# Optimization experiments

Measured on AMD Instinct MI355X. Metric: run time of the kernel, lower is better.

Reference implementation:

```python
import jax, jax.numpy as jnp
import numpy as np

NU, NI = 40000, 60000
N = NU + NI            # total nodes
DF, DL, DI = 1024, 128, 64
E = 1600000            # number of edges
SLOPE = 0.01           # torch leaky_relu default negative slope
EPS = 1e-12            # torch F.normalize eps


def _leaky(v):
    return jnp.where(v > 0, v, SLOPE * v)


def setup_inputs() -> dict:
    key = jax.random.key(0)
    ks = jax.random.split(key, 17)
    s = 0.02  # xavier-ish scale for weights
    return {
        "features": jax.random.normal(ks[0], (NI, DF), jnp.float32),
        "id_embedding": jax.random.normal(ks[1], (N, DI), jnp.float32),
        "preference": jax.random.normal(ks[2], (NU, DL), jnp.float32) * s,
        "mlp_w": jax.random.normal(ks[3], (DL, DF), jnp.float32) * s,
        "mlp_b": jnp.zeros((DL,), jnp.float32),
        "conv1_w": jax.random.normal(ks[4], (DL, DL), jnp.float32) * s,
        "lin1_w": jax.random.normal(ks[5], (DI, DL), jnp.float32) * s,
        "lin1_b": jnp.zeros((DI,), jnp.float32),
        "g1_w": jax.random.normal(ks[6], (DI, DL), jnp.float32) * s,
        "g1_b": jnp.zeros((DI,), jnp.float32),
        "conv2_w": jax.random.normal(ks[7], (DI, DI), jnp.float32) * s,
        "lin2_w": jax.random.normal(ks[8], (DI, DI), jnp.float32) * s,
        "lin2_b": jnp.zeros((DI,), jnp.float32),
        "g2_w": jax.random.normal(ks[9], (DI, DI), jnp.float32) * s,
        "g2_b": jnp.zeros((DI,), jnp.float32),
        "edge_index": jax.random.randint(ks[10], (2, E), 0, N, jnp.int32),
    }


def reference(features, id_embedding, preference, mlp_w, mlp_b,
              conv1_w, lin1_w, lin1_b, g1_w, g1_b,
              conv2_w, lin2_w, lin2_b, g2_w, g2_b, edge_index):
    src, dst = edge_index[0], edge_index[1]

    # MLP on item features, concat with user preference -> [N, DL]
    temp = features @ mlp_w.T + mlp_b
    x = jnp.concatenate([preference, temp], axis=0)
    # row-wise L2 normalize (F.normalize dim=1)
    x = x / jnp.clip(jnp.linalg.norm(x, axis=1, keepdims=True), EPS)

    # ----- layer 1 -----
    xw = x @ conv1_w                                      # [N, DL]
    h = _leaky(jax.ops.segment_sum(xw[src], dst, num_segments=N))
    x_hat = _leaky(x @ lin1_w.T + lin1_b) + id_embedding  # [N, DI]
    x = _leaky(h @ g1_w.T + g1_b + x_hat)                 # [N, DI]

    # ----- layer 2 -----
    xw = x @ conv2_w                                      # [N, DI]
    h = _leaky(jax.ops.segment_sum(xw[src], dst, num_segments=N))
    x_hat = _leaky(x @ lin2_w.T + lin2_b) + id_embedding
    x = _leaky(h @ g2_w.T + g2_b + x_hat)
    return x
```

## Files before the change

kernel.cpp:

```cpp
#include <hip/hip_runtime.h>
#include <hip/hip_bf16.h>

typedef __hip_bfloat16 bf16;
typedef __bf16 bf16x8 __attribute__((ext_vector_type(8)));
typedef float f32x4 __attribute__((ext_vector_type(4)));

#define NU 40000
#define NI 60000
#define NN 100000
#define DF 1024
#define DL 128
#define DI 64
#define NE 1600000
#define CAP 64

__device__ __forceinline__ float leaky(float v) { return v > 0.0f ? v : 0.01f * v; }

__device__ __forceinline__ unsigned short f2b(float f) {
    unsigned u = __builtin_bit_cast(unsigned, f);
    unsigned r = (u + 0x7FFFu + ((u >> 16) & 1u)) >> 16;
    return (unsigned short)r;
}
__device__ __forceinline__ bf16 tobf(float f) {
    unsigned short r = f2b(f);
    return __builtin_bit_cast(bf16, r);
}
__device__ __forceinline__ unsigned pk2(float x, float y) {
    return (unsigned)f2b(x) | ((unsigned)f2b(y) << 16);
}
__device__ __forceinline__ float b2f_lo(unsigned u) { return __builtin_bit_cast(float, u << 16); }
__device__ __forceinline__ float b2f_hi(unsigned u) { return __builtin_bit_cast(float, u & 0xffff0000u); }

template<typename T>
__device__ __forceinline__ void stage8(bf16* dst, const T* src) {
    if constexpr (sizeof(T) == 2) {
        *(uint4*)dst = *(const uint4*)src;
    } else {
        float4 a = *(const float4*)src;
        float4 b = *(const float4*)(src + 4);
        uint2 lo, hi;
        lo.x = pk2(a.x, a.y); lo.y = pk2(a.z, a.w);
        hi.x = pk2(b.x, b.y); hi.y = pk2(b.z, b.w);
        *(uint2*)dst = lo;
        *(uint2*)(dst + 4) = hi;
    }
}
__device__ __forceinline__ void zero8(bf16* dst) {
    uint4 z = {0u, 0u, 0u, 0u};
    *(uint4*)dst = z;
}

__global__ void csr_fill(const int* __restrict__ ei, int* __restrict__ cnt,
                         int* __restrict__ bucket) {
    int e = blockIdx.x * 256 + threadIdx.x;
    if (e >= NE) return;
    int s = ei[e];
    int d = ei[NE + e];
    int p = atomicAdd(&cnt[d], 1);
    if (p < CAP) bucket[d * CAP + p] = s;
}

template<int K, int M>
__global__ void transpose_kernel(const float* __restrict__ W, bf16* __restrict__ Wt) {
    int idx = blockIdx.x * 256 + threadIdx.x;
    if (idx < K * M) {
        int k = idx / M, m = idx % M;
        Wt[m * K + k] = tobf(W[k * M + m]);
    }
}

__global__ void convert_kernel(const float* __restrict__ W, bf16* __restrict__ out) {
    int i = blockIdx.x * 256 + threadIdx.x;
    float4 v = *(const float4*)(W + (size_t)i * 4);
    uint2 p;
    p.x = pk2(v.x, v.y);
    p.y = pk2(v.z, v.w);
    *(uint2*)(out + (size_t)i * 4) = p;
}

__global__ __launch_bounds__(256) void gemm1_kernel(const float* __restrict__ A,
                                                    const bf16* __restrict__ Wb,
                                                    const float* __restrict__ bias,
                                                    bf16* __restrict__ out) {
    __shared__ __align__(16) bf16 As[2][64 * 64];
    __shared__ __align__(16) bf16 Bs[2][128 * 64];
    int t = threadIdx.x;
    int wave = t >> 6, lane = t & 63, q = lane >> 4, l16 = lane & 15;
    int wm = wave >> 1, wn = wave & 1;
    int row0 = blockIdx.x * 64;

    const float* ap[2];
    const bf16* bp[4];
    int aoff[2], boff[4];
    bool aval[2];
    #pragma unroll
    for (int i = 0; i < 2; i++) {
        int slot = t + i * 256;
        int r = slot >> 3, kc = (slot & 7) * 8;
        ap[i] = A + (size_t)(row0 + r) * DF + kc;
        aval[i] = (row0 + r) < NI;
        aoff[i] = r * 64 + (((kc >> 3) ^ (r & 7)) << 3);
    }
    #pragma unroll
    for (int i = 0; i < 4; i++) {
        int slot = t + i * 256;
        int r = slot >> 3, kc = (slot & 7) * 8;
        bp[i] = Wb + (size_t)r * DF + kc;
        boff[i] = r * 64 + (((kc >> 3) ^ (r & 7)) << 3);
    }

    float4 av[2][2];
    uint4 bv[4];
    auto issue = [&](int k0) {
        #pragma unroll
        for (int i = 0; i < 2; i++) {
            if (aval[i]) {
                av[i][0] = *(const float4*)(ap[i] + k0);
                av[i][1] = *(const float4*)(ap[i] + k0 + 4);
            } else {
                av[i][0] = float4{0.f, 0.f, 0.f, 0.f};
                av[i][1] = float4{0.f, 0.f, 0.f, 0.f};
            }
        }
        #pragma unroll
        for (int i = 0; i < 4; i++) bv[i] = *(const uint4*)(bp[i] + k0);
    };
    auto commit = [&](int buf) {
        #pragma unroll
        for (int i = 0; i < 2; i++) {
            uint4 pkd;
            pkd.x = pk2(av[i][0].x, av[i][0].y);
            pkd.y = pk2(av[i][0].z, av[i][0].w);
            pkd.z = pk2(av[i][1].x, av[i][1].y);
            pkd.w = pk2(av[i][1].z, av[i][1].w);
            *(uint4*)(&As[buf][aoff[i]]) = pkd;
        }
        #pragma unroll
        for (int i = 0; i < 4; i++) *(uint4*)(&Bs[buf][boff[i]]) = bv[i];
    };

    f32x4 acc[2][4] = {};
    issue(0);
    commit(0);
    __syncthreads();
    for (int k0i = 0; k0i < 16; k0i++) {
        int buf = k0i & 1;
        if (k0i < 15) issue((k0i + 1) * 64);
        #pragma unroll
        for (int kk = 0; kk < 64; kk += 32) {
            int ch = (kk >> 3) + q;
            int ra = wm * 32 + l16;
            bf16x8 a0 = *(const bf16x8*)&As[buf][ra * 64 + ((ch ^ (ra & 7)) << 3)];
            bf16x8 a1 = *(const bf16x8*)&As[buf][(ra + 16) * 64 + ((ch ^ (ra & 7)) << 3)];
            #pragma unroll
            for (int nt = 0; nt < 4; nt++) {
                int rb = wn * 64 + nt * 16 + l16;
                bf16x8 b = *(const bf16x8*)&Bs[buf][rb * 64 + ((ch ^ (rb & 7)) << 3)];
                acc[0][nt] = __builtin_amdgcn_mfma_f32_16x16x32_bf16(a0, b, acc[0][nt], 0, 0, 0);
                acc[1][nt] = __builtin_amdgcn_mfma_f32_16x16x32_bf16(a1, b, acc[1][nt], 0, 0, 0);
            }
        }
        if (k0i < 15) {
            commit(buf ^ 1);
            __syncthreads();
        }
    }
    #pragma unroll
    for (int mt = 0; mt < 2; mt++) {
        #pragma unroll
        for (int nt = 0; nt < 4; nt++) {
            int col = wn * 64 + nt * 16 + l16;
            float bvv = bias[col];
            #pragma unroll
            for (int r = 0; r < 4; r++) {
                int row = row0 + wm * 32 + mt * 16 + q * 4 + r;
                if (row < NI) out[(size_t)row * DL + col] = tobf(acc[mt][nt][r] + bvv);
            }
        }
    }
}

__global__ __launch_bounds__(256) void norm_kernel(const float* __restrict__ pref,
                                                   const bf16* __restrict__ temp,
                                                   bf16* __restrict__ x0) {
    __shared__ float wsum[4];
    int t = threadIdx.x;
    int g = t >> 7;
    int c = t & 127;
    int row = blockIdx.x * 2 + g;
    float v = (row < NU) ? pref[(size_t)row * DL + c]
                         : (float)temp[(size_t)(row - NU) * DL + c];
    float ss = v * v;
    #pragma unroll
    for (int off = 32; off > 0; off >>= 1) ss += __shfl_down(ss, off);
    int wave = t >> 6;
    if ((t & 63) == 0) wsum[wave] = ss;
    __syncthreads();
    float tot = wsum[g * 2] + wsum[g * 2 + 1];
    float inv = 1.0f / fmaxf(sqrtf(tot), 1e-12f);
    x0[(size_t)row * DL + c] = tobf(v * inv);
}

template<typename WT, int K, int M, int EPI, typename OutT>
__global__ __launch_bounds__(256) void sgemm_kernel(const bf16* __restrict__ A,
                                                    const WT* __restrict__ Wt,
                                                    const float* __restrict__ bias,
                                                    const float* __restrict__ extra,
                                                    OutT* __restrict__ out,
                                                    int nrows) {
    __shared__ __align__(16) bf16 As[128 * K];
    __shared__ __align__(16) bf16 Ws[M * K];
    int t = threadIdx.x;
    int wave = t >> 6, lane = t & 63;
    int q = lane >> 4, l16 = lane & 15;
    int row0 = blockIdx.x * 128;
    constexpr int WSLOT = M * K / 8;
    for (int slot = t; slot < WSLOT; slot += 256)
        stage8(Ws + slot * 8, Wt + (size_t)slot * 8);
    constexpr int SLOTS = 128 * K / 8;
    for (int slot = t; slot < SLOTS; slot += 256) {
        int r = slot / (K / 8);
        int kc = (slot % (K / 8)) * 8;
        int gr = row0 + r;
        if (gr < nrows) *(uint4*)(As + r * K + kc) = *(const uint4*)(A + (size_t)gr * K + kc);
        else            zero8(As + r * K + kc);
    }
    __syncthreads();
    constexpr int NT = M / 16;
    f32x4 acc[2][NT] = {};
    #pragma unroll
    for (int kk = 0; kk < K; kk += 32) {
        bf16x8 a0 = *(const bf16x8*)(As + (wave * 32 + l16) * K + kk + q * 8);
        bf16x8 a1 = *(const bf16x8*)(As + (wave * 32 + 16 + l16) * K + kk + q * 8);
        #pragma unroll
        for (int nt = 0; nt < NT; nt++) {
            bf16x8 b = *(const bf16x8*)(Ws + (nt * 16 + l16) * K + kk + q * 8);
            acc[0][nt] = __builtin_amdgcn_mfma_f32_16x16x32_bf16(a0, b, acc[0][nt], 0, 0, 0);
            acc[1][nt] = __builtin_amdgcn_mfma_f32_16x16x32_bf16(a1, b, acc[1][nt], 0, 0, 0);
        }
    }
    #pragma unroll
    for (int mt = 0; mt < 2; mt++) {
        #pragma unroll
        for (int nt = 0; nt < NT; nt++) {
            int col = nt * 16 + l16;
            float bv = (EPI != 0) ? bias[col] : 0.0f;
            #pragma unroll
            for (int r = 0; r < 4; r++) {
                int row = row0 + wave * 32 + mt * 16 + q * 4 + r;
                if (row < nrows) {
                    float z = acc[mt][nt][r];
                    if (EPI == 1) {
                        z = leaky(z + bv) + extra[(size_t)row * M + col];
                    } else if (EPI == 2) {
                        z = leaky(z + bv + extra[(size_t)row * M + col]);
                    }
                    if constexpr (sizeof(OutT) == 2) out[(size_t)row * M + col] = tobf(z);
                    else                             out[(size_t)row * M + col] = z;
                }
            }
        }
    }
}

template<int D>
__global__ __launch_bounds__(256) void gather_kernel(const bf16* __restrict__ xw,
                                                     const int* __restrict__ cnt,
                                                     const int* __restrict__ bucket,
                                                     bf16* __restrict__ h) {
    constexpr int TPN = D / 4;
    constexpr int GP = 256 / TPN;
    __shared__ int srcs[GP][CAP];
    int g = threadIdx.x / TPN;
    int c = threadIdx.x % TPN;
    int node = blockIdx.x * GP + g;
    int deg = min(cnt[node], CAP);
    for (int i = c; i < deg; i += TPN) srcs[g][i] = bucket[node * CAP + i];
    __syncthreads();
    const uint2* x2 = (const uint2*)xw;
    float s0 = 0.0f, s1 = 0.0f, s2 = 0.0f, s3 = 0.0f;
    for (int i = 0; i < deg; i++) {
        int s = srcs[g][i];
        uint2 v = x2[(size_t)s * (D / 4) + c];
        s0 += b2f_lo(v.x); s1 += b2f_hi(v.x);
        s2 += b2f_lo(v.y); s3 += b2f_hi(v.y);
    }
    uint2 o;
    o.x = pk2(leaky(s0), leaky(s1));
    o.y = pk2(leaky(s2), leaky(s3));
    *(uint2*)(h + (size_t)node * D + c * 4) = o;
}

extern "C" void kernel_launch(void* const* d_in, const int* in_sizes, int n_in,
                              void* d_out, int out_size, void* d_ws, size_t ws_size,
                              hipStream_t stream) {
    const void* p[16];
    for (int i = 0; i < 16 && i < n_in; i++) p[i] = d_in[i];
    if (n_in == 16) {
        int n8192 = 0, n4096 = 0, n64 = 0;
        const int idx64[4] = {7, 9, 12, 14};
        const int idx4096[3] = {10, 11, 13};
        for (int i = 0; i < 16; i++) {
            switch (in_sizes[i]) {
                case 61440000: p[0] = d_in[i]; break;
                case 6400000:  p[1] = d_in[i]; break;
                case 5120000:  p[2] = d_in[i]; break;
                case 131072:   p[3] = d_in[i]; break;
                case 128:      p[4] = d_in[i]; break;
                case 16384:    p[5] = d_in[i]; break;
                case 8192:     p[n8192++ ? 8 : 6] = d_in[i]; break;
                case 64:       if (n64 < 4) p[idx64[n64++]] = d_in[i]; break;
                case 4096:     if (n4096 < 3) p[idx4096[n4096++]] = d_in[i]; break;
                case 3200000:  p[15] = d_in[i]; break;
                default: break;
            }
        }
    }
    const float* features = (const float*)p[0];
    const float* id_emb   = (const float*)p[1];
    const float* pref     = (const float*)p[2];
    const float* mlp_w    = (const float*)p[3];
    const float* mlp_b    = (const float*)p[4];
    const float* conv1_w  = (const float*)p[5];
    const float* lin1_w   = (const float*)p[6];
    const float* lin1_b   = (const float*)p[7];
    const float* g1_w     = (const float*)p[8];
    const float* g1_b     = (const float*)p[9];
    const float* conv2_w  = (const float*)p[10];
    const float* lin2_w   = (const float*)p[11];
    const float* lin2_b   = (const float*)p[12];
    const float* g2_w     = (const float*)p[13];
    const float* g2_b     = (const float*)p[14];
    const int*   ei       = (const int*)p[15];

    char* wsp = (char*)d_ws;
    size_t off = 0;
    auto alloc = [&](size_t bytes) {
        void* ptr = wsp + off;
        off += (bytes + 255) & ~(size_t)255;
        return ptr;
    };
    void* regA = alloc((size_t)NN * DL * 2);
    void* regB = alloc((size_t)NN * DL * 2);
    void* regC = alloc((size_t)NN * DL * 2);
    int*  cnt    = (int*) alloc((size_t)NN * 4);
    int*  bucket = (int*) alloc((size_t)NN * CAP * 4);
    bf16* c1t    = (bf16*)alloc((size_t)DL * DL * 2);
    bf16* c2t    = (bf16*)alloc((size_t)DI * DI * 2);

    bf16*  temp = (bf16*)regA;
    bf16*  h1   = (bf16*)regA;
    bf16*  h2   = (bf16*)regA;
    bf16*  x0   = (bf16*)regB;
    bf16*  xw2  = (bf16*)regB;
    bf16*  mwb  = (bf16*)regC;
    bf16*  xw1  = (bf16*)regC;
    float* xhat = (float*)regC;
    bf16*  x1   = (bf16*)d_out;
    float* out  = (float*)d_out;

    hipMemsetAsync(cnt, 0, (size_t)NN * 4, stream);
    csr_fill<<<NE / 256, 256, 0, stream>>>(ei, cnt, bucket);

    transpose_kernel<DL, DL><<<(DL * DL + 255) / 256, 256, 0, stream>>>(conv1_w, c1t);
    transpose_kernel<DI, DI><<<(DI * DI + 255) / 256, 256, 0, stream>>>(conv2_w, c2t);
    convert_kernel<<<(DL * DF) / 1024, 256, 0, stream>>>(mlp_w, mwb);

    gemm1_kernel<<<(NI + 63) / 64, 256, 0, stream>>>(features, mwb, mlp_b, temp);
    norm_kernel<<<NN / 2, 256, 0, stream>>>(pref, temp, x0);

    const int SG = (NN + 127) / 128;
    sgemm_kernel<bf16, DL, DL, 0, bf16><<<SG, 256, 0, stream>>>(x0, c1t, nullptr, nullptr, xw1, NN);
    gather_kernel<DL><<<NN / 8, 256, 0, stream>>>(xw1, cnt, bucket, h1);
    sgemm_kernel<float, DL, DI, 1, float><<<SG, 256, 0, stream>>>(x0, lin1_w, lin1_b, id_emb, xhat, NN);
    sgemm_kernel<float, DL, DI, 2, bf16><<<SG, 256, 0, stream>>>(h1, g1_w, g1_b, xhat, x1, NN);
    sgemm_kernel<float, DI, DI, 1, float><<<SG, 256, 0, stream>>>(x1, lin2_w, lin2_b, id_emb, xhat, NN);
    sgemm_kernel<bf16, DI, DI, 0, bf16><<<SG, 256, 0, stream>>>(x1, c2t, nullptr, nullptr, xw2, NN);
    gather_kernel<DI><<<NN / 16, 256, 0, stream>>>(xw2, cnt, bucket, h2);
    sgemm_kernel<float, DI, DI, 2, float><<<SG, 256, 0, stream>>>(h2, g2_w, g2_b, xhat, out, NN);
}
```

Baseline: 806.9 us.

## Fuse sibling small GEMMs, merge weight prep, widen gather loads

```diff
diff --git a/kernel.cpp b/kernel.cpp
--- a/kernel.cpp
+++ b/kernel.cpp
@@ -31,25 +31,6 @@
 __device__ __forceinline__ float b2f_lo(unsigned u) { return __builtin_bit_cast(float, u << 16); }
 __device__ __forceinline__ float b2f_hi(unsigned u) { return __builtin_bit_cast(float, u & 0xffff0000u); }
 
-template<typename T>
-__device__ __forceinline__ void stage8(bf16* dst, const T* src) {
-    if constexpr (sizeof(T) == 2) {
-        *(uint4*)dst = *(const uint4*)src;
-    } else {
-        float4 a = *(const float4*)src;
-        float4 b = *(const float4*)(src + 4);
-        uint2 lo, hi;
-        lo.x = pk2(a.x, a.y); lo.y = pk2(a.z, a.w);
-        hi.x = pk2(b.x, b.y); hi.y = pk2(b.z, b.w);
-        *(uint2*)dst = lo;
-        *(uint2*)(dst + 4) = hi;
-    }
-}
-__device__ __forceinline__ void zero8(bf16* dst) {
-    uint4 z = {0u, 0u, 0u, 0u};
-    *(uint4*)dst = z;
-}
-
 __global__ void csr_fill(const int* __restrict__ ei, int* __restrict__ cnt,
                          int* __restrict__ bucket) {
     int e = blockIdx.x * 256 + threadIdx.x;
@@ -60,22 +41,43 @@
     if (p < CAP) bucket[d * CAP + p] = s;
 }
 
-template<int K, int M>
-__global__ void transpose_kernel(const float* __restrict__ W, bf16* __restrict__ Wt) {
-    int idx = blockIdx.x * 256 + threadIdx.x;
-    if (idx < K * M) {
-        int k = idx / M, m = idx % M;
-        Wt[m * K + k] = tobf(W[k * M + m]);
-    }
-}
-
-__global__ void convert_kernel(const float* __restrict__ W, bf16* __restrict__ out) {
-    int i = blockIdx.x * 256 + threadIdx.x;
-    float4 v = *(const float4*)(W + (size_t)i * 4);
-    uint2 p;
-    p.x = pk2(v.x, v.y);
-    p.y = pk2(v.z, v.w);
-    *(uint2*)(out + (size_t)i * 4) = p;
+__global__ __launch_bounds__(256) void prep_kernel(
+        const float* __restrict__ mlp_w, const float* __restrict__ conv1_w,
+        const float* __restrict__ conv2_w, const float* __restrict__ lin1_w,
+        const float* __restrict__ g1_w, const float* __restrict__ lin2_w,
+        const float* __restrict__ g2_w,
+        bf16* __restrict__ mwb, bf16* __restrict__ c1t, bf16* __restrict__ c2t,
+        bf16* __restrict__ l1b, bf16* __restrict__ g1b,
+        bf16* __restrict__ l2b, bf16* __restrict__ g2b) {
+    int b = blockIdx.x, t = threadIdx.x;
+    if (b < 128) {
+        int i = b * 256 + t;
+        float4 v = *(const float4*)(mlp_w + (size_t)i * 4);
+        uint2 pk;
+        pk.x = pk2(v.x, v.y);
+        pk.y = pk2(v.z, v.w);
+        *(uint2*)(mwb + (size_t)i * 4) = pk;
+    } else if (b < 192) {
+        int i = (b - 128) * 256 + t;
+        int k = i >> 7, m = i & 127;
+        c1t[m * 128 + k] = tobf(conv1_w[i]);
+    } else if (b < 208) {
+        int i = (b - 192) * 256 + t;
+        int k = i >> 6, m = i & 63;
+        c2t[m * 64 + k] = tobf(conv2_w[i]);
+    } else if (b < 240) {
+        int i = (b - 208) * 256 + t;
+        l1b[i] = tobf(lin1_w[i]);
+    } else if (b < 272) {
+        int i = (b - 240) * 256 + t;
+        g1b[i] = tobf(g1_w[i]);
+    } else if (b < 288) {
+        int i = (b - 272) * 256 + t;
+        l2b[i] = tobf(lin2_w[i]);
+    } else {
+        int i = (b - 288) * 256 + t;
+        g2b[i] = tobf(g2_w[i]);
+    }
 }
 
 __global__ __launch_bounds__(256) void gemm1_kernel(const float* __restrict__ A,
@@ -201,62 +203,81 @@
     x0[(size_t)row * DL + c] = tobf(v * inv);
 }
 
-template<typename WT, int K, int M, int EPI, typename OutT>
-__global__ __launch_bounds__(256) void sgemm_kernel(const bf16* __restrict__ A,
-                                                    const WT* __restrict__ Wt,
-                                                    const float* __restrict__ bias,
-                                                    const float* __restrict__ extra,
-                                                    OutT* __restrict__ out,
-                                                    int nrows) {
-    __shared__ __align__(16) bf16 As[128 * K];
-    __shared__ __align__(16) bf16 Ws[M * K];
+template<int K, int M1, int EPI1, typename Out1T, int M2, int EPI2, typename Out2T>
+__global__ __launch_bounds__(256) void fgemm_kernel(
+        const bf16* __restrict__ A,
+        const bf16* __restrict__ W1, const float* __restrict__ b1,
+        const float* __restrict__ e1, Out1T* __restrict__ o1,
+        const bf16* __restrict__ W2, const float* __restrict__ b2,
+        const float* __restrict__ e2, Out2T* __restrict__ o2,
+        int nrows) {
+    constexpr int NT1 = M1 / 16;
+    constexpr int NT2 = (M2 > 0) ? (M2 / 16) : 0;
     int t = threadIdx.x;
-    int wave = t >> 6, lane = t & 63;
-    int q = lane >> 4, l16 = lane & 15;
-    int row0 = blockIdx.x * 128;
-    constexpr int WSLOT = M * K / 8;
-    for (int slot = t; slot < WSLOT; slot += 256)
-        stage8(Ws + slot * 8, Wt + (size_t)slot * 8);
-    constexpr int SLOTS = 128 * K / 8;
-    for (int slot = t; slot < SLOTS; slot += 256) {
-        int r = slot / (K / 8);
-        int kc = (slot % (K / 8)) * 8;
-        int gr = row0 + r;
-        if (gr < nrows) *(uint4*)(As + r * K + kc) = *(const uint4*)(A + (size_t)gr * K + kc);
-        else            zero8(As + r * K + kc);
-    }
-    __syncthreads();
-    constexpr int NT = M / 16;
-    f32x4 acc[2][NT] = {};
+    int wave = t >> 6, lane = t & 63, q = lane >> 4, l16 = lane & 15;
+    int rbase = blockIdx.x * 128 + wave * 32;
+    int r0 = rbase + l16, r1 = r0 + 16;
+    const bf16* a0p = A + (size_t)r0 * K + q * 8;
+    const bf16* a1p = A + (size_t)r1 * K + q * 8;
+    bool v0 = r0 < nrows, v1 = r1 < nrows;
+    f32x4 acc1[2][NT1] = {};
+    f32x4 acc2[2][NT2 ? NT2 : 1] = {};
+    const bf16x8 zz = {};
     #pragma unroll
     for (int kk = 0; kk < K; kk += 32) {
-        bf16x8 a0 = *(const bf16x8*)(As + (wave * 32 + l16) * K + kk + q * 8);
-        bf16x8 a1 = *(const bf16x8*)(As + (wave * 32 + 16 + l16) * K + kk + q * 8);
-        #pragma unroll
-        for (int nt = 0; nt < NT; nt++) {
-            bf16x8 b = *(const bf16x8*)(Ws + (nt * 16 + l16) * K + kk + q * 8);
-            acc[0][nt] = __builtin_amdgcn_mfma_f32_16x16x32_bf16(a0, b, acc[0][nt], 0, 0, 0);
-            acc[1][nt] = __builtin_amdgcn_mfma_f32_16x16x32_bf16(a1, b, acc[1][nt], 0, 0, 0);
+        bf16x8 a0 = v0 ? *(const bf16x8*)(a0p + kk) : zz;
+        bf16x8 a1 = v1 ? *(const bf16x8*)(a1p + kk) : zz;
+        #pragma unroll
+        for (int nt = 0; nt < NT1; nt++) {
+            bf16x8 b = *(const bf16x8*)(W1 + (size_t)(nt * 16 + l16) * K + kk + q * 8);
+            acc1[0][nt] = __builtin_amdgcn_mfma_f32_16x16x32_bf16(a0, b, acc1[0][nt], 0, 0, 0);
+            acc1[1][nt] = __builtin_amdgcn_mfma_f32_16x16x32_bf16(a1, b, acc1[1][nt], 0, 0, 0);
+        }
+        if constexpr (NT2 > 0) {
+            #pragma unroll
+            for (int nt = 0; nt < NT2; nt++) {
+                bf16x8 b = *(const bf16x8*)(W2 + (size_t)(nt * 16 + l16) * K + kk + q * 8);
+                acc2[0][nt] = __builtin_amdgcn_mfma_f32_16x16x32_bf16(a0, b, acc2[0][nt], 0, 0, 0);
+                acc2[1][nt] = __builtin_amdgcn_mfma_f32_16x16x32_bf16(a1, b, acc2[1][nt], 0, 0, 0);
+            }
         }
     }
     #pragma unroll
     for (int mt = 0; mt < 2; mt++) {
         #pragma unroll
-        for (int nt = 0; nt < NT; nt++) {
+        for (int nt = 0; nt < NT1; nt++) {
             int col = nt * 16 + l16;
-            float bv = (EPI != 0) ? bias[col] : 0.0f;
+            float bv = (EPI1 != 0) ? b1[col] : 0.0f;
             #pragma unroll
             for (int r = 0; r < 4; r++) {
-                int row = row0 + wave * 32 + mt * 16 + q * 4 + r;
+                int row = rbase + mt * 16 + q * 4 + r;
                 if (row < nrows) {
-                    float z = acc[mt][nt][r];
-                    if (EPI == 1) {
-                        z = leaky(z + bv) + extra[(size_t)row * M + col];
-                    } else if (EPI == 2) {
-                        z = leaky(z + bv + extra[(size_t)row * M + col]);
+                    float z = acc1[mt][nt][r];
+                    if constexpr (EPI1 == 1) z = leaky(z + bv) + e1[(size_t)row * M1 + col];
+                    else if constexpr (EPI1 == 2) z = leaky(z + bv + e1[(size_t)row * M1 + col]);
+                    if constexpr (sizeof(Out1T) == 2) o1[(size_t)row * M1 + col] = tobf(z);
+                    else                              o1[(size_t)row * M1 + col] = z;
+                }
+            }
+        }
+    }
+    if constexpr (NT2 > 0) {
+        #pragma unroll
+        for (int mt = 0; mt < 2; mt++) {
+            #pragma unroll
+            for (int nt = 0; nt < NT2; nt++) {
+                int col = nt * 16 + l16;
+                float bv = (EPI2 != 0) ? b2[col] : 0.0f;
+                #pragma unroll
+                for (int r = 0; r < 4; r++) {
+                    int row = rbase + mt * 16 + q * 4 + r;
+                    if (row < nrows) {
+                        float z = acc2[mt][nt][r];
+                        if constexpr (EPI2 == 1) z = leaky(z + bv) + e2[(size_t)row * M2 + col];
+                        else if constexpr (EPI2 == 2) z = leaky(z + bv + e2[(size_t)row * M2 + col]);
+                        if constexpr (sizeof(Out2T) == 2) o2[(size_t)row * M2 + col] = tobf(z);
+                        else                              o2[(size_t)row * M2 + col] = z;
                     }
-                    if constexpr (sizeof(OutT) == 2) out[(size_t)row * M + col] = tobf(z);
-                    else                             out[(size_t)row * M + col] = z;
                 }
             }
         }
@@ -268,27 +289,43 @@
                                                      const int* __restrict__ cnt,
                                                      const int* __restrict__ bucket,
                                                      bf16* __restrict__ h) {
-    constexpr int TPN = D / 4;
+    constexpr int TPN = D / 8;
     constexpr int GP = 256 / TPN;
-    __shared__ int srcs[GP][CAP];
+    __shared__ int srcs[GP][CAP + 1];
     int g = threadIdx.x / TPN;
     int c = threadIdx.x % TPN;
     int node = blockIdx.x * GP + g;
     int deg = min(cnt[node], CAP);
     for (int i = c; i < deg; i += TPN) srcs[g][i] = bucket[node * CAP + i];
     __syncthreads();
-    const uint2* x2 = (const uint2*)xw;
-    float s0 = 0.0f, s1 = 0.0f, s2 = 0.0f, s3 = 0.0f;
-    for (int i = 0; i < deg; i++) {
-        int s = srcs[g][i];
-        uint2 v = x2[(size_t)s * (D / 4) + c];
-        s0 += b2f_lo(v.x); s1 += b2f_hi(v.x);
-        s2 += b2f_lo(v.y); s3 += b2f_hi(v.y);
-    }
-    uint2 o;
+    const uint4* x4 = (const uint4*)xw;
+    float s0 = 0, s1 = 0, s2 = 0, s3 = 0, s4 = 0, s5 = 0, s6 = 0, s7 = 0;
+    int i = 0;
+    for (; i + 2 <= deg; i += 2) {
+        uint4 va = x4[(size_t)srcs[g][i] * (D / 8) + c];
+        uint4 vb = x4[(size_t)srcs[g][i + 1] * (D / 8) + c];
+        s0 += b2f_lo(va.x); s1 += b2f_hi(va.x);
+        s2 += b2f_lo(va.y); s3 += b2f_hi(va.y);
+        s4 += b2f_lo(va.z); s5 += b2f_hi(va.z);
+        s6 += b2f_lo(va.w); s7 += b2f_hi(va.w);
+        s0 += b2f_lo(vb.x); s1 += b2f_hi(vb.x);
+        s2 += b2f_lo(vb.y); s3 += b2f_hi(vb.y);
+        s4 += b2f_lo(vb.z); s5 += b2f_hi(vb.z);
+        s6 += b2f_lo(vb.w); s7 += b2f_hi(vb.w);
+    }
+    if (i < deg) {
+        uint4 va = x4[(size_t)srcs[g][i] * (D / 8) + c];
+        s0 += b2f_lo(va.x); s1 += b2f_hi(va.x);
+        s2 += b2f_lo(va.y); s3 += b2f_hi(va.y);
+        s4 += b2f_lo(va.z); s5 += b2f_hi(va.z);
+        s6 += b2f_lo(va.w); s7 += b2f_hi(va.w);
+    }
+    uint4 o;
     o.x = pk2(leaky(s0), leaky(s1));
     o.y = pk2(leaky(s2), leaky(s3));
-    *(uint2*)(h + (size_t)node * D + c * 4) = o;
+    o.z = pk2(leaky(s4), leaky(s5));
+    o.w = pk2(leaky(s6), leaky(s7));
+    *(uint4*)(h + (size_t)node * D + c * 8) = o;
 }
 
 extern "C" void kernel_launch(void* const* d_in, const int* in_sizes, int n_in,
@@ -343,39 +380,44 @@
     void* regA = alloc((size_t)NN * DL * 2);
     void* regB = alloc((size_t)NN * DL * 2);
     void* regC = alloc((size_t)NN * DL * 2);
+    void* regD = alloc((size_t)NN * DI * 4);
     int*  cnt    = (int*) alloc((size_t)NN * 4);
     int*  bucket = (int*) alloc((size_t)NN * CAP * 4);
     bf16* c1t    = (bf16*)alloc((size_t)DL * DL * 2);
     bf16* c2t    = (bf16*)alloc((size_t)DI * DI * 2);
-
-    bf16*  temp = (bf16*)regA;
-    bf16*  h1   = (bf16*)regA;
-    bf16*  h2   = (bf16*)regA;
-    bf16*  x0   = (bf16*)regB;
-    bf16*  xw2  = (bf16*)regB;
-    bf16*  mwb  = (bf16*)regC;
-    bf16*  xw1  = (bf16*)regC;
-    float* xhat = (float*)regC;
-    bf16*  x1   = (bf16*)d_out;
-    float* out  = (float*)d_out;
+    bf16* l1b    = (bf16*)alloc((size_t)DI * DL * 2);
+    bf16* g1b    = (bf16*)alloc((size_t)DI * DL * 2);
+    bf16* l2b    = (bf16*)alloc((size_t)DI * DI * 2);
+    bf16* g2b    = (bf16*)alloc((size_t)DI * DI * 2);
+
+    bf16*  temp  = (bf16*)regA;
+    bf16*  h1    = (bf16*)regA;
+    bf16*  h2    = (bf16*)regA;
+    bf16*  x0    = (bf16*)regB;
+    bf16*  xw2   = (bf16*)regB;
+    bf16*  mwb   = (bf16*)regC;
+    bf16*  xw1   = (bf16*)regC;
+    float* xhat  = (float*)regD;
+    bf16*  x1    = (bf16*)d_out;
+    float* out   = (float*)d_out;
 
     hipMemsetAsync(cnt, 0, (size_t)NN * 4, stream);
     csr_fill<<<NE / 256, 256, 0, stream>>>(ei, cnt, bucket);
-
-    transpose_kernel<DL, DL><<<(DL * DL + 255) / 256, 256, 0, stream>>>(conv1_w, c1t);
-    transpose_kernel<DI, DI><<<(DI * DI + 255) / 256, 256, 0, stream>>>(conv2_w, c2t);
-    convert_kernel<<<(DL * DF) / 1024, 256, 0, stream>>>(mlp_w, mwb);
+    prep_kernel<<<304, 256, 0, stream>>>(mlp_w, conv1_w, conv2_w, lin1_w, g1_w,
+                                         lin2_w, g2_w, mwb, c1t, c2t, l1b, g1b, l2b, g2b);
 
     gemm1_kernel<<<(NI + 63) / 64, 256, 0, stream>>>(features, mwb, mlp_b, temp);
     norm_kernel<<<NN / 2, 256, 0, stream>>>(pref, temp, x0);
 
     const int SG = (NN + 127) / 128;
-    sgemm_kernel<bf16, DL, DL, 0, bf16><<<SG, 256, 0, stream>>>(x0, c1t, nullptr, nullptr, xw1, NN);
-    gather_kernel<DL><<<NN / 8, 256, 0, stream>>>(xw1, cnt, bucket, h1);
-    sgemm_kernel<float, DL, DI, 1, float><<<SG, 256, 0, stream>>>(x0, lin1_w, lin1_b, id_emb, xhat, NN);
-    sgemm_kernel<float, DL, DI, 2, bf16><<<SG, 256, 0, stream>>>(h1, g1_w, g1_b, xhat, x1, NN);
-    sgemm_kernel<float, DI, DI, 1, float><<<SG, 256, 0, stream>>>(x1, lin2_w, lin2_b, id_emb, xhat, NN);
-    sgemm_kernel<bf16, DI, DI, 0, bf16><<<SG, 256, 0, stream>>>(x1, c2t, nullptr, nullptr, xw2, NN);
-    gather_kernel<DI><<<NN / 16, 256, 0, stream>>>(xw2, cnt, bucket, h2);
-    sgemm_kernel<float, DI, DI, 2, float><<<SG, 256, 0, stream>>>(h2, g2_w, g2_b, xhat, out, NN);
-}
+    fgemm_kernel<DL, DL, 0, bf16, DI, 1, float><<<SG, 256, 0, stream>>>(
+        x0, c1t, nullptr, nullptr, xw1, l1b, lin1_b, id_emb, xhat, NN);
+    gather_kernel<DL><<<NN / 16, 256, 0, stream>>>(xw1, cnt, bucket, h1);
+    fgemm_kernel<DL, DI, 2, bf16, 0, 0, bf16><<<SG, 256, 0, stream>>>(
+        h1, g1b, g1_b, xhat, x1, nullptr, nullptr, nullptr, nullptr, NN);
+    fgemm_kernel<DI, DI, 0, bf16, DI, 1, float><<<SG, 256, 0, stream>>>(
+        x1, c2t, nullptr, nullptr, xw2, l2b, lin2_b, id_emb, xhat, NN);
+    gather_kernel<DI><<<NN / 32, 256, 0, stream>>>(xw2, cnt, bucket, h2);
+    fgemm_kernel<DI, DI, 2, float, 0, 0, float><<<SG, 256, 0, stream>>>(
+        h2, g2b, g2_b, xhat, out, nullptr, nullptr, nullptr, nullptr, NN);
+}
```

Result: faster. 780.1 us (-3.3%).
